# Performance work log

Measured on AMD Instinct MI355X. Metric: run time of the kernel, lower is better.

The kernel has to match this reference:

```python
import jax, jax.numpy as jnp
import numpy as np

DIL = 2      # dilation of deformable depthwise conv (padding == dilation -> same size)
EPS = 1e-5   # BatchNorm eps
B, C, O, G, H, W = 4, 256, 256, 64, 64, 64


def conv2d(x, w, padding, dilation=1):
    return jax.lax.conv_general_dilated(
        x, w, window_strides=(1, 1), padding=[(padding, padding)] * 2,
        rhs_dilation=(dilation, dilation),
        dimension_numbers=("NCHW", "OIHW", "NCHW"))


def bn_inf(x, gamma, beta, mean, var):
    scale = (gamma / jnp.sqrt(var + EPS))[None, :, None, None]
    return (x - mean[None, :, None, None]) * scale + beta[None, :, None, None]


def bilinear_gather(xt, ys, xs):
    # xt: [B,H,W,C]; ys, xs: [B,K,H,W] float sample coords. Zero padding outside.
    Bb, Hh, Ww, Cc = xt.shape
    y0 = jnp.floor(ys)
    x0 = jnp.floor(xs)
    wy = (ys - y0)[..., None]
    wx = (xs - x0)[..., None]
    bidx = jnp.arange(Bb)[:, None, None, None]

    def gather(yi, xi):
        valid = (yi >= 0) & (yi < Hh) & (xi >= 0) & (xi < Ww)
        yc = jnp.clip(yi, 0, Hh - 1).astype(jnp.int32)
        xc = jnp.clip(xi, 0, Ww - 1).astype(jnp.int32)
        val = xt[bidx, yc, xc]            # [B,K,H,W,C]
        return val * valid[..., None].astype(xt.dtype)

    v00 = gather(y0, x0)
    v01 = gather(y0, x0 + 1)
    v10 = gather(y0 + 1, x0)
    v11 = gather(y0 + 1, x0 + 1)
    return (v00 * (1 - wy) * (1 - wx) + v01 * (1 - wy) * wx
            + v10 * wy * (1 - wx) + v11 * wy * wx)


def setup_inputs() -> dict:
    key = jax.random.key(0)
    ks = jax.random.split(key, 12)
    inp = {
        "x": jax.random.normal(ks[0], (B, C, H, W), jnp.float32),
        "grad_feats": jax.random.normal(ks[1], (B, G, H, W), jnp.float32),
        # offset block: conv3x3(G->18) + BN + ReLU
        "off_w": jax.random.normal(ks[2], (18, G, 3, 3), jnp.float32) / np.sqrt(G * 9),
        "off_gamma": 1.0 + 0.1 * jax.random.normal(ks[3], (18,), jnp.float32),
        "off_beta": 0.1 * jax.random.normal(ks[4], (18,), jnp.float32),
        "off_mean": 0.1 * jax.random.normal(ks[5], (18,), jnp.float32),
        "off_var": jax.random.uniform(ks[6], (18,), jnp.float32, 0.5, 1.5),
        # deformable separable conv: depthwise 3x3 (per-channel) then pointwise 1x1, no bias
        "dw_w": jax.random.normal(ks[7], (C, 3, 3), jnp.float32) / 3.0,
        "pw_w": jax.random.normal(ks[8], (O, C), jnp.float32) / np.sqrt(C),
        # output BN
        "bn_gamma": 1.0 + 0.1 * jax.random.normal(ks[9], (O,), jnp.float32),
        "bn_beta": 0.1 * jax.random.normal(ks[10], (O,), jnp.float32),
        "bn_mean": 0.1 * jax.random.normal(ks[11], (O,), jnp.float32),
        "bn_var": jnp.ones((O,), jnp.float32),
    }
    return inp


def reference(x, grad_feats, off_w, off_gamma, off_beta, off_mean, off_var,
              dw_w, pw_w, bn_gamma, bn_beta, bn_mean, bn_var):
    Bb, Cc, Hh, Ww = x.shape
    # offset block: conv3x3 + BN + ReLU -> [B,18,H,W]
    off = jax.nn.relu(bn_inf(conv2d(grad_feats, off_w, 1),
                             off_gamma, off_beta, off_mean, off_var))
    off = off.reshape(Bb, 9, 2, Hh, Ww)
    dy, dx = off[:, :, 0], off[:, :, 1]                     # [B,9,H,W]
    # base kernel grid: padding == dilation so tap offsets are (kh-1)*DIL
    kk = (jnp.arange(3, dtype=jnp.float32) - 1.0) * DIL
    ky = jnp.repeat(kk, 3)                                   # [9] row offsets
    kx = jnp.tile(kk, 3)                                     # [9] col offsets
    gy = jnp.arange(Hh, dtype=jnp.float32)[None, None, :, None] + ky[None, :, None, None] + dy
    gx = jnp.arange(Ww, dtype=jnp.float32)[None, None, None, :] + kx[None, :, None, None] + dx
    samp = bilinear_gather(x.transpose(0, 2, 3, 1), gy, gx)  # [B,9,H,W,C]
    out = jnp.einsum("bkhwc,ck->bchw", samp, dw_w.reshape(Cc, 9))   # depthwise
    out = jnp.einsum("bchw,oc->bohw", out, pw_w)                    # pointwise 1x1
    out = jax.nn.relu(bn_inf(out, bn_gamma, bn_beta, bn_mean, bn_var))
    return out
```

## Files before the change

kernel.cpp:

```cpp
#include <hip/hip_runtime.h>
#include <stdint.h>

#define Bn 4
#define Cn 256
#define On 256
#define Gn 64
#define Hn 64
#define Wn 64
#define HWn 4096
#define EPSf 1e-5f

#define WS_XT    0u
#define WS_OFF   8388608u
#define WS_PWB   9568256u

typedef __attribute__((ext_vector_type(8))) short short8;
typedef __attribute__((ext_vector_type(4))) float f4;

__device__ __forceinline__ unsigned int bfround(float f) {
    unsigned int u = __float_as_uint(f);
    u += 0x7FFFu + ((u >> 16) & 1u);
    return u >> 16;
}
__device__ __forceinline__ float blo(unsigned u) { return __uint_as_float(u << 16); }
__device__ __forceinline__ float bhi(unsigned u) { return __uint_as_float(u & 0xFFFF0000u); }

__global__ __launch_bounds__(256, 4) void k_prep(const float* __restrict__ x,
                                                 const float* __restrict__ pw_w,
                                                 const float* __restrict__ off_w,
                                                 const float* __restrict__ gf,
                                                 const float* __restrict__ og,
                                                 const float* __restrict__ obt,
                                                 const float* __restrict__ om,
                                                 const float* __restrict__ ov,
                                                 char* __restrict__ ws)
{
    __shared__ float smem[4680];
    int tid = threadIdx.x, bid = blockIdx.x;

    if (bid < 1024) {
        unsigned short* xt = (unsigned short*)(ws + WS_XT);
        int pt = bid & 63, ct = (bid >> 6) & 3, b = bid >> 8;
        int p0 = pt * 64, c0 = ct * 64;
        const f4* x4 = (const f4*)(x + (size_t)b * Cn * HWn);
        #pragma unroll
        for (int it = 0; it < 4; ++it) {
            int v = it * 256 + tid;
            int ci = v >> 4, pj = v & 15;
            f4 f = __builtin_nontemporal_load(&x4[(size_t)(c0 + ci) * 1024 + (p0 >> 2) + pj]);
            smem[ci * 65 + pj * 4 + 0] = f[0];
            smem[ci * 65 + pj * 4 + 1] = f[1];
            smem[ci * 65 + pj * 4 + 2] = f[2];
            smem[ci * 65 + pj * 4 + 3] = f[3];
        }
        __syncthreads();
        unsigned short* xtb = xt + (size_t)b * HWn * Cn;
        #pragma unroll
        for (int it = 0; it < 2; ++it) {
            int u = it * 256 + tid;
            int pi = u >> 3, cj = u & 7;
            float f[8];
            #pragma unroll
            for (int j = 0; j < 8; ++j)
                f[j] = smem[(cj * 8 + j) * 65 + pi];
            uint4 pk;
            pk.x = bfround(f[0]) | (bfround(f[1]) << 16);
            pk.y = bfround(f[2]) | (bfround(f[3]) << 16);
            pk.z = bfround(f[4]) | (bfround(f[5]) << 16);
            pk.w = bfround(f[6]) | (bfround(f[7]) << 16);
            *(uint4*)(xtb + (size_t)(p0 + pi) * Cn + c0 + cj * 8) = pk;
        }
        return;
    }
    if (bid < 1056) {
        unsigned short* pwb = (unsigned short*)(ws + WS_PWB);
        const float4* p4 = (const float4*)pw_w;
        uint2* o2 = (uint2*)pwb;
        int base = (bid - 1024) * 512;
        #pragma unroll
        for (int i = 0; i < 2; ++i) {
            int id2 = base + i * 256 + tid;
            float4 f = p4[id2];
            uint2 pk;
            pk.x = bfround(f.x) | (bfround(f.y) << 16);
            pk.y = bfround(f.z) | (bfround(f.w) << 16);
            o2[id2] = pk;
        }
        return;
    }
    {
        float* off = (float*)(ws + WS_OFF);
        int idx = bid - 1056;
        int h = idx & 63, b = idx >> 6;
        int lane = tid & 63;
        int wvU = __builtin_amdgcn_readfirstlane(tid >> 6);

        float acc[18];
        #pragma unroll
        for (int ch = 0; ch < 18; ++ch) acc[ch] = 0.f;

        const float* gfb = gf + (size_t)b * Gn * HWn;
        for (int gi = 0; gi < 16; ++gi) {
            int g = wvU * 16 + gi;
            const float* gfg = gfb + (size_t)g * HWn;
            float rv[3], su[3], sd[3];
            #pragma unroll
            for (int r = 0; r < 3; ++r) {
                int y = h - 1 + r;
                rv[r] = ((unsigned)y < 64u) ? gfg[y * 64 + lane] : 0.f;
            }
            #pragma unroll
            for (int r = 0; r < 3; ++r) {
                float u = __shfl_up(rv[r], 1);   su[r] = (lane == 0)  ? 0.f : u;
                float d = __shfl_down(rv[r], 1); sd[r] = (lane == 63) ? 0.f : d;
            }
            #pragma unroll
            for (int ty = 0; ty < 3; ++ty) {
                const float* wb = off_w + g * 9 + ty * 3;
                #pragma unroll
                for (int ch = 0; ch < 18; ++ch)
                    acc[ch] += wb[ch * 576 + 0] * su[ty]
                             + wb[ch * 576 + 1] * rv[ty]
                             + wb[ch * 576 + 2] * sd[ty];
            }
        }

        #pragma unroll
        for (int ch = 0; ch < 18; ++ch)
            smem[(wvU * 18 + ch) * 65 + lane] = acc[ch];
        __syncthreads();

        float* obp = off + (size_t)(b * HWn + h * 64) * 18;
        for (int i = tid; i < 1152; i += 256) {
            int w = i / 18, ch = i - w * 18;
            float v = smem[ch * 65 + w] + smem[(18 + ch) * 65 + w]
                    + smem[(36 + ch) * 65 + w] + smem[(54 + ch) * 65 + w];
            float s = og[ch] * rsqrtf(ov[ch] + EPSf);
            v = (v - om[ch]) * s + obt[ch];
            obp[i] = v > 0.f ? v : 0.f;
        }
    }
}

#define TLD 264
__global__ __launch_bounds__(512, 4) void k_fuse(float* __restrict__ out,
                                                 const float* __restrict__ dw_w,
                                                 const float* __restrict__ bg,
                                                 const float* __restrict__ bb,
                                                 const float* __restrict__ bm,
                                                 const float* __restrict__ bv,
                                                 const char* __restrict__ ws)
{
    const unsigned short* __restrict__ xt  = (const unsigned short*)(ws + WS_XT);
    const unsigned short* __restrict__ pwb = (const unsigned short*)(ws + WS_PWB);
    const float* __restrict__ off = (const float*)(ws + WS_OFF);
    __shared__ float smeta[288 * 8];
    __shared__ float sdw[9 * 256];
    __shared__ unsigned short tl[32 * TLD];

    int bid = blockIdx.x;
    int xcd = bid & 7, slot = bid >> 3;
    int b = xcd >> 1;
    int h = ((xcd & 1) << 5) | (slot >> 1);
    int w0 = (slot & 1) << 5;
    int tid = threadIdx.x;

    for (int i = tid; i < 2304; i += 512) {
        int k = i >> 8, c = i & 255;
        sdw[i] = dw_w[c * 9 + k];
    }

    if (tid < 288) {
        int k = tid >> 5, wl = tid & 31;
        int w = w0 + wl;
        int kyi = k / 3, kxi = k - kyi * 3;
        const float* op = off + ((size_t)(b * HWn + h * 64 + w)) * 18 + 2 * k;
        float dy = op[0], dx = op[1];
        float gy = (float)(h + (kyi - 1) * 2) + dy;
        float gx = (float)(w + (kxi - 1) * 2) + dx;
        float fy = floorf(gy), fx = floorf(gx);
        float wy = gy - fy, wx = gx - fx;
        int y0 = (int)fy, x0 = (int)fx;
        int y1 = y0 + 1, x1 = x0 + 1;
        float m00 = ((unsigned)y0 < 64u && (unsigned)x0 < 64u) ? 1.f : 0.f;
        float m01 = ((unsigned)y0 < 64u && (unsigned)x1 < 64u) ? 1.f : 0.f;
        float m10 = ((unsigned)y1 < 64u && (unsigned)x0 < 64u) ? 1.f : 0.f;
        float m11 = ((unsigned)y1 < 64u && (unsigned)x1 < 64u) ? 1.f : 0.f;
        int y0c = min(max(y0, 0), 63), y1c = min(max(y1, 0), 63);
        int x0c = min(max(x0, 0), 63), x1c = min(max(x1, 0), 63);
        float4 mw;
        mw.x = (1.f - wy) * (1.f - wx) * m00;
        mw.y = (1.f - wy) * wx * m01;
        mw.z = wy * (1.f - wx) * m10;
        mw.w = wy * wx * m11;
        float4 mo;
        mo.x = __int_as_float((y0c * 64 + x0c) << 9);
        mo.y = __int_as_float((y0c * 64 + x1c) << 9);
        mo.z = __int_as_float((y1c * 64 + x0c) << 9);
        mo.w = __int_as_float((y1c * 64 + x1c) << 9);
        float4* s4w = (float4*)smeta;
        s4w[(k * 32 + wl) * 2] = mw;
        s4w[(k * 32 + wl) * 2 + 1] = mo;
    }
    __syncthreads();

    int lane = tid & 63, wave = tid >> 6;
    int half = lane >> 5, c8 = lane & 31;
    int c0 = c8 * 8;

    const char* xb = (const char*)(xt + (size_t)b * HWn * Cn);
    int laneByte = c8 * 16;
    const float4* s4 = (const float4*)smeta;
    #pragma unroll
    for (int iter = 0; iter < 2; ++iter) {
        int wl = iter * 16 + wave * 2 + half;
        float acc[8];
        #pragma unroll
        for (int j = 0; j < 8; ++j) acc[j] = 0.f;
        #pragma unroll 1
        for (int k = 0; k < 9; ++k) {
            float4 mw = s4[(k * 32 + wl) * 2];
            float4 mo = s4[(k * 32 + wl) * 2 + 1];
            float4 d0 = *(const float4*)(&sdw[k * 256 + c0]);
            float4 d1 = *(const float4*)(&sdw[k * 256 + c0 + 4]);
            uint4 qA = *(const uint4*)(xb + __float_as_int(mo.x) + laneByte);
            uint4 qB = *(const uint4*)(xb + __float_as_int(mo.y) + laneByte);
            uint4 qC = *(const uint4*)(xb + __float_as_int(mo.z) + laneByte);
            uint4 qD = *(const uint4*)(xb + __float_as_int(mo.w) + laneByte);
            const unsigned* uA = (const unsigned*)&qA;
            const unsigned* uB = (const unsigned*)&qB;
            const unsigned* uC = (const unsigned*)&qC;
            const unsigned* uD = (const unsigned*)&qD;
            const float* dk0 = (const float*)&d0;
            const float* dk1 = (const float*)&d1;
            #pragma unroll
            for (int j = 0; j < 4; ++j) {
                const float* dkj = (j < 2) ? dk0 : dk1;
                int jj = (j & 1) * 2;
                float sl = mw.x * blo(uA[j]) + mw.y * blo(uB[j]) + mw.z * blo(uC[j]) + mw.w * blo(uD[j]);
                float sh = mw.x * bhi(uA[j]) + mw.y * bhi(uB[j]) + mw.z * bhi(uC[j]) + mw.w * bhi(uD[j]);
                acc[2 * j]     += sl * dkj[jj];
                acc[2 * j + 1] += sh * dkj[jj + 1];
            }
        }
        uint4 pk;
        pk.x = bfround(acc[0]) | (bfround(acc[1]) << 16);
        pk.y = bfround(acc[2]) | (bfround(acc[3]) << 16);
        pk.z = bfround(acc[4]) | (bfround(acc[5]) << 16);
        pk.w = bfround(acc[6]) | (bfround(acc[7]) << 16);
        *(uint4*)(&tl[wl * TLD + c0]) = pk;
    }
    __syncthreads();

    int m0 = wave * 32;
    int row = lane & 15, quad = lane >> 4;
    f4 acc[2][2];
    #pragma unroll
    for (int i = 0; i < 2; ++i)
        #pragma unroll
        for (int j = 0; j < 2; ++j)
            acc[i][j] = (f4){0.f, 0.f, 0.f, 0.f};

    #pragma unroll 2
    for (int kq = 0; kq < 8; ++kq) {
        int kk = kq * 32 + quad * 8;
        short8 a[2], bf[2];
        #pragma unroll
        for (int mt = 0; mt < 2; ++mt)
            a[mt] = *(const short8*)(pwb + (size_t)(m0 + mt * 16 + row) * Cn + kk);
        #pragma unroll
        for (int nt = 0; nt < 2; ++nt)
            bf[nt] = *(const short8*)(&tl[(nt * 16 + row) * TLD + kk]);
        #pragma unroll
        for (int mt = 0; mt < 2; ++mt)
            #pragma unroll
            for (int nt = 0; nt < 2; ++nt)
                acc[mt][nt] = __builtin_amdgcn_mfma_f32_16x16x32_bf16(a[mt], bf[nt], acc[mt][nt], 0, 0, 0);
    }

    float* obp = out + (size_t)b * On * HWn + h * 64 + w0;
    #pragma unroll
    for (int mt = 0; mt < 2; ++mt) {
        #pragma unroll
        for (int r = 0; r < 4; ++r) {
            int o = m0 + mt * 16 + quad * 4 + r;
            float s = bg[o] * rsqrtf(bv[o] + EPSf);
            float sh = bb[o] - bm[o] * s;
            #pragma unroll
            for (int nt = 0; nt < 2; ++nt) {
                float v = acc[mt][nt][r] * s + sh;
                v = v > 0.f ? v : 0.f;
                __builtin_nontemporal_store(v, &obp[(size_t)o * HWn + nt * 16 + row]);
            }
        }
    }
}

extern "C" void kernel_launch(void* const* d_in, const int* in_sizes, int n_in,
                              void* d_out, int out_size, void* d_ws, size_t ws_size,
                              hipStream_t stream)
{
    const float* x     = (const float*)d_in[0];
    const float* gf    = (const float*)d_in[1];
    const float* off_w = (const float*)d_in[2];
    const float* og    = (const float*)d_in[3];
    const float* ob    = (const float*)d_in[4];
    const float* om    = (const float*)d_in[5];
    const float* ov    = (const float*)d_in[6];
    const float* dw_w  = (const float*)d_in[7];
    const float* pw_w  = (const float*)d_in[8];
    const float* bg    = (const float*)d_in[9];
    const float* bb    = (const float*)d_in[10];
    const float* bm    = (const float*)d_in[11];
    const float* bv    = (const float*)d_in[12];
    float* out = (float*)d_out;
    char* ws = (char*)d_ws;

    hipLaunchKernelGGL(k_prep, dim3(1312), dim3(256), 0, stream,
                       x, pw_w, off_w, gf, og, ob, om, ov, ws);
    hipLaunchKernelGGL(k_fuse, dim3(512), dim3(512), 0, stream,
                       out, dw_w, bg, bb, bm, bv, ws);
}
```

Before: 140.1 us.

## Merge prep and fuse kernels into one cooperative kernel with grid sync

Replaces the two-kernel launch (prep, then fused deformable conv plus pointwise GEMM) with a single cooperative kernel of 512 blocks that runs the prep work and then does a grid-wide sync before the fuse phase. In prep, 256 blocks compute the offset conv and the other 256 each transpose four tiles of x to bf16, with some also converting pw_w. The goal is to remove the second kernel launch and the gap between kernels. In exchange it adds grid.sync overhead and packs the prep work onto fewer, larger blocks. If the cooperative launch fails, it falls back to the old two-kernel path.

```diff
diff --git a/kernel.cpp b/kernel.cpp
--- a/kernel.cpp
+++ b/kernel.cpp
@@ -1,5 +1,8 @@
 #include <hip/hip_runtime.h>
+#include <hip/hip_cooperative_groups.h>
 #include <stdint.h>
+
+namespace cg = cooperative_groups;
 
 #define Bn 4
 #define Cn 256
@@ -24,6 +27,287 @@
 }
 __device__ __forceinline__ float blo(unsigned u) { return __uint_as_float(u << 16); }
 __device__ __forceinline__ float bhi(unsigned u) { return __uint_as_float(u & 0xFFFF0000u); }
+
+#define TLD 264
+
+
+__global__ __launch_bounds__(512, 4) void k_all(const float* __restrict__ x,
+                                                const float* __restrict__ pw_w,
+                                                const float* __restrict__ off_w,
+                                                const float* __restrict__ gf,
+                                                const float* __restrict__ og,
+                                                const float* __restrict__ obt,
+                                                const float* __restrict__ om,
+                                                const float* __restrict__ ov,
+                                                const float* __restrict__ dw_w,
+                                                const float* __restrict__ bg,
+                                                const float* __restrict__ bb,
+                                                const float* __restrict__ bm,
+                                                const float* __restrict__ bv,
+                                                float* __restrict__ out,
+                                                char* __restrict__ ws)
+{
+    cg::grid_group grid = cg::this_grid();
+    __shared__ __align__(16) char sbuf[31872];
+    int tid = threadIdx.x, bid = blockIdx.x;
+    int lane = tid & 63;
+
+    if (bid < 256) {
+        float* sred = (float*)sbuf;
+        float* off = (float*)(ws + WS_OFF);
+        int h = bid & 63, b = bid >> 6;
+        int wvU = __builtin_amdgcn_readfirstlane(tid >> 6);
+
+        float acc[18];
+        #pragma unroll
+        for (int ch = 0; ch < 18; ++ch) acc[ch] = 0.f;
+
+        const float* gfb = gf + (size_t)b * Gn * HWn;
+        #pragma unroll 2
+        for (int gi = 0; gi < 8; ++gi) {
+            int g = wvU * 8 + gi;
+            const float* gfg = gfb + (size_t)g * HWn;
+            float rv[3], su[3], sd[3];
+            #pragma unroll
+            for (int r = 0; r < 3; ++r) {
+                int y = h - 1 + r;
+                rv[r] = ((unsigned)y < 64u) ? gfg[y * 64 + lane] : 0.f;
+            }
+            #pragma unroll
+            for (int r = 0; r < 3; ++r) {
+                float u = __shfl_up(rv[r], 1);   su[r] = (lane == 0)  ? 0.f : u;
+                float d = __shfl_down(rv[r], 1); sd[r] = (lane == 63) ? 0.f : d;
+            }
+            #pragma unroll
+            for (int ty = 0; ty < 3; ++ty) {
+                const float* wb = off_w + g * 9 + ty * 3;
+                #pragma unroll
+                for (int ch = 0; ch < 18; ++ch)
+                    acc[ch] += wb[ch * 576 + 0] * su[ty]
+                             + wb[ch * 576 + 1] * rv[ty]
+                             + wb[ch * 576 + 2] * sd[ty];
+            }
+        }
+
+        if (wvU < 4) {
+            #pragma unroll
+            for (int ch = 0; ch < 18; ++ch)
+                sred[(wvU * 18 + ch) * 65 + lane] = acc[ch];
+        }
+        __syncthreads();
+        if (wvU >= 4) {
+            #pragma unroll
+            for (int ch = 0; ch < 18; ++ch)
+                sred[((wvU - 4) * 18 + ch) * 65 + lane] += acc[ch];
+        }
+        __syncthreads();
+
+        float* obp = off + (size_t)(b * HWn + h * 64) * 18;
+        for (int i = tid; i < 1152; i += 512) {
+            int w = i / 18, ch = i - w * 18;
+            float v = sred[ch * 65 + w] + sred[(18 + ch) * 65 + w]
+                    + sred[(36 + ch) * 65 + w] + sred[(54 + ch) * 65 + w];
+            float s = og[ch] * rsqrtf(ov[ch] + EPSf);
+            v = (v - om[ch]) * s + obt[ch];
+            obp[i] = v > 0.f ? v : 0.f;
+        }
+    } else {
+        float* tile = (float*)sbuf;
+        unsigned short* xt = (unsigned short*)(ws + WS_XT);
+        int idx = bid - 256;
+        #pragma unroll 1
+        for (int tt = 0; tt < 4; ++tt) {
+            int t = idx * 4 + tt;
+            int pt = t & 63, ct = (t >> 6) & 3, b = t >> 8;
+            int p0 = pt * 64, c0 = ct * 64;
+            const f4* x4 = (const f4*)(x + (size_t)b * Cn * HWn);
+            #pragma unroll
+            for (int it = 0; it < 2; ++it) {
+                int v = it * 512 + tid;
+                int ci = v >> 4, pj = v & 15;
+                f4 f = __builtin_nontemporal_load(&x4[(size_t)(c0 + ci) * 1024 + (p0 >> 2) + pj]);
+                tile[ci * 65 + pj * 4 + 0] = f[0];
+                tile[ci * 65 + pj * 4 + 1] = f[1];
+                tile[ci * 65 + pj * 4 + 2] = f[2];
+                tile[ci * 65 + pj * 4 + 3] = f[3];
+            }
+            __syncthreads();
+            unsigned short* xtb = xt + (size_t)b * HWn * Cn;
+            {
+                int pi = tid >> 3, cj = tid & 7;
+                float f[8];
+                #pragma unroll
+                for (int j = 0; j < 8; ++j)
+                    f[j] = tile[(cj * 8 + j) * 65 + pi];
+                uint4 pk;
+                pk.x = bfround(f[0]) | (bfround(f[1]) << 16);
+                pk.y = bfround(f[2]) | (bfround(f[3]) << 16);
+                pk.z = bfround(f[4]) | (bfround(f[5]) << 16);
+                pk.w = bfround(f[6]) | (bfround(f[7]) << 16);
+                *(uint4*)(xtb + (size_t)(p0 + pi) * Cn + c0 + cj * 8) = pk;
+            }
+            __syncthreads();
+        }
+        if (idx < 32) {
+            unsigned short* pwb = (unsigned short*)(ws + WS_PWB);
+            const float4* p4 = (const float4*)pw_w;
+            uint2* o2 = (uint2*)pwb;
+            int id2 = idx * 512 + tid;
+            float4 f = p4[id2];
+            uint2 pk;
+            pk.x = bfround(f.x) | (bfround(f.y) << 16);
+            pk.y = bfround(f.z) | (bfround(f.w) << 16);
+            o2[id2] = pk;
+        }
+    }
+
+    __threadfence();
+    grid.sync();
+
+    {
+        const unsigned short* xt  = (const unsigned short*)(ws + WS_XT);
+        const unsigned short* pwb = (const unsigned short*)(ws + WS_PWB);
+        const float* off = (const float*)(ws + WS_OFF);
+        float* smw = (float*)sbuf;
+        unsigned* scoord = (unsigned*)(sbuf + 4608);
+        float* sdw = (float*)(sbuf + 5760);
+        unsigned short* tl = (unsigned short*)(sbuf + 14976);
+
+        int xcd = bid & 7, slot = bid >> 3;
+        int b = xcd >> 1;
+        int h = ((xcd & 1) << 5) | (slot >> 1);
+        int w0 = (slot & 1) << 5;
+
+        for (int i = tid; i < 2304; i += 512) {
+            int k = i >> 8, c = i & 255;
+            sdw[i] = dw_w[c * 9 + k];
+        }
+
+        if (tid < 288) {
+            int k = tid >> 5, wl = tid & 31;
+            int w = w0 + wl;
+            int kyi = k / 3, kxi = k - kyi * 3;
+            const float* op = off + ((size_t)(b * HWn + h * 64 + w)) * 18 + 2 * k;
+            float dy = op[0], dx = op[1];
+            float gy = (float)(h + (kyi - 1) * 2) + dy;
+            float gx = (float)(w + (kxi - 1) * 2) + dx;
+            float fy = floorf(gy), fx = floorf(gx);
+            float wy = gy - fy, wx = gx - fx;
+            int y0 = (int)fy, x0 = (int)fx;
+            int y1 = y0 + 1, x1 = x0 + 1;
+            float m00 = ((unsigned)y0 < 64u && (unsigned)x0 < 64u) ? 1.f : 0.f;
+            float m01 = ((unsigned)y0 < 64u && (unsigned)x1 < 64u) ? 1.f : 0.f;
+            float m10 = ((unsigned)y1 < 64u && (unsigned)x0 < 64u) ? 1.f : 0.f;
+            float m11 = ((unsigned)y1 < 64u && (unsigned)x1 < 64u) ? 1.f : 0.f;
+            int y0c = min(max(y0, 0), 63), y1c = min(max(y1, 0), 63);
+            int x0c = min(max(x0, 0), 63), x1c = min(max(x1, 0), 63);
+            float4 mw;
+            mw.x = (1.f - wy) * (1.f - wx) * m00;
+            mw.y = (1.f - wy) * wx * m01;
+            mw.z = wy * (1.f - wx) * m10;
+            mw.w = wy * wx * m11;
+            ((float4*)smw)[k * 32 + wl] = mw;
+            int p00 = y0c * 64 + x0c;
+            int p11 = y1c * 64 + x1c;
+            scoord[k * 32 + wl] = (unsigned)(p00 | (p11 << 12));
+        }
+        __syncthreads();
+
+        int wave = tid >> 6;
+        int half = lane >> 5, c8 = lane & 31;
+        int c0 = c8 * 8;
+
+        const char* xb = (const char*)(xt + (size_t)b * HWn * Cn);
+        int laneByte = c8 * 16;
+        #pragma unroll
+        for (int iter = 0; iter < 2; ++iter) {
+            int wl = iter * 16 + wave * 2 + half;
+            float acc[8];
+            #pragma unroll
+            for (int j = 0; j < 8; ++j) acc[j] = 0.f;
+            #pragma unroll 1
+            for (int k = 0; k < 9; ++k) {
+                float4 mw = ((const float4*)smw)[k * 32 + wl];
+                unsigned pc = scoord[k * 32 + wl];
+                int p00 = pc & 0xFFF;
+                int p11 = (pc >> 12) & 0xFFF;
+                int p01 = (p00 & ~63) | (p11 & 63);
+                int p10 = (p11 & ~63) | (p00 & 63);
+                float4 d0 = *(const float4*)(&sdw[k * 256 + c0]);
+                float4 d1 = *(const float4*)(&sdw[k * 256 + c0 + 4]);
+                uint4 qA = *(const uint4*)(xb + (p00 << 9) + laneByte);
+                uint4 qB = *(const uint4*)(xb + (p01 << 9) + laneByte);
+                uint4 qC = *(const uint4*)(xb + (p10 << 9) + laneByte);
+                uint4 qD = *(const uint4*)(xb + (p11 << 9) + laneByte);
+                const unsigned* uA = (const unsigned*)&qA;
+                const unsigned* uB = (const unsigned*)&qB;
+                const unsigned* uC = (const unsigned*)&qC;
+                const unsigned* uD = (const unsigned*)&qD;
+                const float* dk0 = (const float*)&d0;
+                const float* dk1 = (const float*)&d1;
+                #pragma unroll
+                for (int j = 0; j < 4; ++j) {
+                    const float* dkj = (j < 2) ? dk0 : dk1;
+                    int jj = (j & 1) * 2;
+                    float sl = mw.x * blo(uA[j]) + mw.y * blo(uB[j]) + mw.z * blo(uC[j]) + mw.w * blo(uD[j]);
+                    float sh = mw.x * bhi(uA[j]) + mw.y * bhi(uB[j]) + mw.z * bhi(uC[j]) + mw.w * bhi(uD[j]);
+                    acc[2 * j]     += sl * dkj[jj];
+                    acc[2 * j + 1] += sh * dkj[jj + 1];
+                }
+            }
+            uint4 pk;
+            pk.x = bfround(acc[0]) | (bfround(acc[1]) << 16);
+            pk.y = bfround(acc[2]) | (bfround(acc[3]) << 16);
+            pk.z = bfround(acc[4]) | (bfround(acc[5]) << 16);
+            pk.w = bfround(acc[6]) | (bfround(acc[7]) << 16);
+            *(uint4*)(&tl[wl * TLD + c0]) = pk;
+        }
+        __syncthreads();
+
+        int m0 = wave * 32;
+        int row = lane & 15, quad = lane >> 4;
+        f4 acc[2][2];
+        #pragma unroll
+        for (int i = 0; i < 2; ++i)
+            #pragma unroll
+            for (int j = 0; j < 2; ++j)
+                acc[i][j] = (f4){0.f, 0.f, 0.f, 0.f};
+
+        #pragma unroll 2
+        for (int kq = 0; kq < 8; ++kq) {
+            int kk = kq * 32 + quad * 8;
+            short8 a[2], bf[2];
+            #pragma unroll
+            for (int mt = 0; mt < 2; ++mt)
+                a[mt] = *(const short8*)(pwb + (size_t)(m0 + mt * 16 + row) * Cn + kk);
+            #pragma unroll
+            for (int nt = 0; nt < 2; ++nt)
+                bf[nt] = *(const short8*)(&tl[(nt * 16 + row) * TLD + kk]);
+            #pragma unroll
+            for (int mt = 0; mt < 2; ++mt)
+                #pragma unroll
+                for (int nt = 0; nt < 2; ++nt)
+                    acc[mt][nt] = __builtin_amdgcn_mfma_f32_16x16x32_bf16(a[mt], bf[nt], acc[mt][nt], 0, 0, 0);
+        }
+
+        float* obp = out + (size_t)b * On * HWn + h * 64 + w0;
+        #pragma unroll
+        for (int mt = 0; mt < 2; ++mt) {
+            #pragma unroll
+            for (int r = 0; r < 4; ++r) {
+                int o = m0 + mt * 16 + quad * 4 + r;
+                float s = bg[o] * rsqrtf(bv[o] + EPSf);
+                float sh = bb[o] - bm[o] * s;
+                #pragma unroll
+                for (int nt = 0; nt < 2; ++nt) {
+                    float v = acc[mt][nt][r] * s + sh;
+                    v = v > 0.f ? v : 0.f;
+                    __builtin_nontemporal_store(v, &obp[(size_t)o * HWn + nt * 16 + row]);
+                }
+            }
+        }
+    }
+}
 
 __global__ __launch_bounds__(256, 4) void k_prep(const float* __restrict__ x,
                                                  const float* __restrict__ pw_w,
@@ -142,7 +426,6 @@
     }
 }
 
-#define TLD 264
 __global__ __launch_bounds__(512, 4) void k_fuse(float* __restrict__ out,
                                                  const float* __restrict__ dw_w,
                                                  const float* __restrict__ bg,
@@ -316,8 +599,17 @@
     float* out = (float*)d_out;
     char* ws = (char*)d_ws;
 
-    hipLaunchKernelGGL(k_prep, dim3(1312), dim3(256), 0, stream,
-                       x, pw_w, off_w, gf, og, ob, om, ov, ws);
-    hipLaunchKernelGGL(k_fuse, dim3(512), dim3(512), 0, stream,
-                       out, dw_w, bg, bb, bm, bv, ws);
+    void* args[] = { (void*)&x, (void*)&pw_w, (void*)&off_w, (void*)&gf,
+                     (void*)&og, (void*)&ob, (void*)&om, (void*)&ov,
+                     (void*)&dw_w, (void*)&bg, (void*)&bb, (void*)&bm, (void*)&bv,
+                     (void*)&out, (void*)&ws };
+    hipError_t err = hipLaunchCooperativeKernel((const void*)k_all, dim3(512), dim3(512),
+                                                args, 0, stream);
+    if (err != hipSuccess) {
+        (void)hipGetLastError();
+        hipLaunchKernelGGL(k_prep, dim3(1312), dim3(256), 0, stream,
+                           x, pw_w, off_w, gf, og, ob, om, ov, ws);
+        hipLaunchKernelGGL(k_fuse, dim3(512), dim3(512), 0, stream,
+                           out, dw_w, bg, bb, bm, bv, ws);
+    }
 }
```

Measured after the change: 293.1 us. 109% more time.
